# Kernel tuning notes

Hardware: AMD Instinct MI355X
Metric: run time of the kernel (lower is better)

## Reference

```python
import jax, jax.numpy as jnp
import numpy as np

N_NODES = 50000
N_EDGES = 800000
MUL = 32      # node feature multiplicity (32x0e)
A = 8         # node attr multiplicity (8x0e)
VE = 4        # edge attr multiplicity (4x0e)
FC_IN = 16    # edge_scalars dim (fc_neurons[0])
FC_H = 64     # fc hidden (fc_neurons[1])
W_NUMEL = MUL * VE  # tp.weight_numel for 'uvu' instruction = 128
NUM_NEIGHBORS = 16
N_LAYERS = 2


def fctp(x, y, w):
    # FullyConnectedTensorProduct on pure scalars: x[n,U], y[n,V], w[U,V,K]
    U, V = w.shape[0], w.shape[1]
    return jnp.einsum('nu,nv,uvk->nk', x, y, w) / np.float32(np.sqrt(U * V))


def tp_uvu(x, y, w):
    # 'uvu' TensorProduct with per-edge weights: x[e,U], y[e,V], w[e,U,V]
    V = y.shape[1]
    return jnp.einsum('eu,ev,euv->eu', x, y, w) / np.float32(np.sqrt(V))


def conv_layer(node_in, node_attr, edge_src, edge_dst, edge_attr, edge_scalars,
               sc_w, lin1_w, lin2_w, alpha_w, sce_w, fc_w0, fc_w1):
    n_nodes = node_in.shape[0]
    # per-edge weight generation (FullyConnectedNet with sin activation)
    h = jnp.sin(edge_scalars @ fc_w0 / np.float32(np.sqrt(FC_IN)))          # [E, FC_H]
    w = (h @ fc_w1 / np.float32(np.sqrt(FC_H))).reshape(-1, MUL, VE)        # [E, MUL, VE]
    # self connection + lin1
    node_sc = fctp(node_in, node_attr, sc_w)                                # [N, K]
    x = fctp(node_in, node_attr, lin1_w)                                    # [N, MUL]
    # gather -> tensor product -> scatter-add
    edge_features = tp_uvu(x[edge_src], edge_attr, w)                       # [E, MUL]
    node_features = jax.ops.segment_sum(edge_features, edge_dst,
                                        num_segments=n_nodes)
    node_features = node_features / np.float32(np.sqrt(NUM_NEIGHBORS))      # [N, MUL]
    node_conv = fctp(node_features, node_attr, lin2_w)                      # [N, K]
    alpha = fctp(node_features, node_attr, alpha_w)                         # [N, 1]
    # output_mask is all ones for scalar outputs -> alpha = 1 - 1 + alpha*1
    node_out = node_sc + alpha * node_conv
    edge_out = edge_attr + fctp(edge_features, edge_attr, sce_w) / np.float32(np.sqrt(NUM_NEIGHBORS))
    return node_out, edge_out


def setup_inputs() -> dict:
    key = jax.random.key(0)
    ks = jax.random.split(key, 13)
    L = N_LAYERS
    return {
        'node_features': jax.random.normal(ks[0], (N_NODES, MUL), jnp.float32),
        'node_attr':     jax.random.normal(ks[1], (N_NODES, A), jnp.float32),
        'edge_src':      jax.random.randint(ks[2], (N_EDGES,), 0, N_NODES),
        'edge_dst':      jax.random.randint(ks[3], (N_EDGES,), 0, N_NODES),
        'edge_attr':     jax.random.normal(ks[4], (N_EDGES, VE), jnp.float32),
        'edge_scalars':  jax.random.normal(ks[5], (N_EDGES, FC_IN), jnp.float32),
        # stacked per-layer parameters
        'sc_w':    jax.random.normal(ks[6],  (L, MUL, A, MUL), jnp.float32),
        'lin1_w':  jax.random.normal(ks[7],  (L, MUL, A, MUL), jnp.float32),
        'lin2_w':  jax.random.normal(ks[8],  (L, MUL, A, MUL), jnp.float32),
        'alpha_w': 0.1 * jax.random.normal(ks[9], (L, MUL, A, 1), jnp.float32),
        'sce_w':   jax.random.normal(ks[10], (L, MUL, VE, VE), jnp.float32),
        'fc_w0':   jax.random.normal(ks[11], (L, FC_IN, FC_H), jnp.float32),
        'fc_w1':   jax.random.normal(ks[12], (L, FC_H, W_NUMEL), jnp.float32),
    }


def reference(node_features, node_attr, edge_src, edge_dst, edge_attr, edge_scalars,
              sc_w, lin1_w, lin2_w, alpha_w, sce_w, fc_w0, fc_w1):
    nf, ea = node_features, edge_attr
    for l in range(N_LAYERS):
        nf, ea = conv_layer(nf, node_attr, edge_src, edge_dst, ea, edge_scalars,
                            sc_w[l], lin1_w[l], lin2_w[l], alpha_w[l],
                            sce_w[l], fc_w0[l], fc_w1[l])
        if l < N_LAYERS - 1:
            nf = jnp.sin(nf)  # Gate over even scalars == elementwise sin
    return nf, ea
```

## Files before the change

### kernel.cpp

```cpp
#include <hip/hip_runtime.h>
#include <hip/hip_bf16.h>


namespace {
constexpr int NN = 50000;
constexpr int NE = 800000;
constexpr int SCAN_BLOCKS = 196;

constexpr long OFF_NF   = 0;
constexpr long OFF_W0P  = 1600000;
constexpr long OFF_W2P  = 1602048;
constexpr long OFF_WNP  = 1610240;
constexpr long OFF_OFF  = 1638912;
constexpr long OFF_CUR  = 1688913;
constexpr long OFF_PERM = 1738913;
constexpr long OFF_BSUM = 2538913;
constexpr long OFF_EF   = 2539172;
}

typedef __attribute__((ext_vector_type(8))) short short8;
typedef __attribute__((ext_vector_type(4))) float f32x4;
typedef __attribute__((ext_vector_type(2))) float f32x2;
typedef f32x2 __attribute__((may_alias)) f32x2a;
typedef unsigned int   __attribute__((may_alias)) u32a;
typedef unsigned short __attribute__((may_alias)) u16a;
typedef float          __attribute__((may_alias)) f32a;

__device__ __forceinline__ float us2f(unsigned int u) {
    unsigned int x = u << 16; float f;
    __builtin_memcpy(&f, &x, sizeof(f));
    return f;
}
__device__ __forceinline__ unsigned short f2us(float f) {
    __hip_bfloat16 h = __float2bfloat16(f);
    unsigned short s;
    __builtin_memcpy(&s, &h, sizeof(s));
    return s;
}
__device__ __forceinline__ f32x2 mk2(float a, float b) {
    f32x2 r; r[0] = a; r[1] = b; return r;
}
__device__ __forceinline__ f32x2 pkfma(f32x2 a, f32x2 b, f32x2 c) {
#if __has_builtin(__builtin_elementwise_fma)
    return __builtin_elementwise_fma(a, b, c);
#else
    f32x2 r; r[0] = fmaf(a[0], b[0], c[0]); r[1] = fmaf(a[1], b[1], c[1]);
    return r;
#endif
}

__global__ __launch_bounds__(256) void k_hist(
        const int* __restrict__ dst, int* __restrict__ cnt,
        const float* __restrict__ f0, const float* __restrict__ f1,
        const float* __restrict__ l1w, const float* __restrict__ scw,
        const float* __restrict__ l2w, const float* __restrict__ aw,
        unsigned short* __restrict__ w0p, unsigned short* __restrict__ w2p,
        unsigned short* __restrict__ wnp) {
    int i = blockIdx.x * 256 + threadIdx.x;
    if (i < NE) atomicAdd(&cnt[dst[i]], 1);
    if (i < 4096) {
        int l = i >> 11, r = i & 2047;
        int nt = r >> 9, lane = (r >> 3) & 63, ii = r & 7;
        int k = (lane >> 4) * 8 + ii;
        int j = nt * 16 + (lane & 15);
        float v = (k < 16) ? 0.25f * f0[l * 1024 + k * 64 + j] : 0.f;
        w0p[i] = f2us(v);
    }
    if (i < 16384) {
        int l = i >> 13, r = i & 8191;
        int g = r >> 9;
        int kt = g >> 1, nt = g & 1;
        int lane = (r >> 3) & 63, ii = r & 7;
        int K = kt * 32 + (lane >> 4) * 8 + ii;
        int j = K >> 2, v = K & 3;
        int u = nt * 16 + (lane & 15);
        w2p[i] = f2us(f1[l * 8192 + j * 128 + u * 4 + v]);
    }
    if (i < 57344) {
        int l = i / 28672, r = i % 28672;
        int tile = r >> 12;
        int r2 = r & 4095;
        int kt = r2 >> 9, lane = (r2 >> 3) & 63, ii = r2 & 7;
        int k = kt * 32 + (lane >> 4) * 8 + ii;
        int u = k >> 3, v = k & 7;
        int col = lane & 15;
        int uvb = l * 8192 + (u * 8 + v) * 32;
        float val;
        if (tile < 2)      val = l1w[uvb + tile * 16 + col];
        else if (tile < 4) val = scw[uvb + (tile - 2) * 16 + col];
        else if (tile < 6) val = l2w[uvb + (tile - 4) * 16 + col];
        else               val = (col == 0) ? aw[l * 256 + u * 8 + v] : 0.f;
        wnp[i] = f2us(val);
    }
}

__global__ __launch_bounds__(256) void k_scan1(const int* __restrict__ cnt,
                                               int* __restrict__ bsum) {
    __shared__ int s[256];
    int t = threadIdx.x;
    int i = blockIdx.x * 256 + t;
    s[t] = (i < NN) ? cnt[i] : 0;
    __syncthreads();
    for (int d = 128; d > 0; d >>= 1) {
        if (t < d) s[t] += s[t + d];
        __syncthreads();
    }
    if (t == 0) bsum[blockIdx.x] = s[0];
}

__global__ __launch_bounds__(256) void k_scan2(int* __restrict__ bsum) {
    __shared__ int s[256];
    int t = threadIdx.x;
    int v = (t < SCAN_BLOCKS) ? bsum[t] : 0;
    s[t] = v; __syncthreads();
    for (int d = 1; d < 256; d <<= 1) {
        int x = (t >= d) ? s[t - d] : 0;
        __syncthreads();
        s[t] += x;
        __syncthreads();
    }
    if (t < SCAN_BLOCKS) bsum[t] = s[t] - v;
}

__global__ __launch_bounds__(256) void k_scan3(
        const int* __restrict__ cnt, const int* __restrict__ bsum,
        int* __restrict__ off, int* __restrict__ cur) {
    __shared__ int s[256];
    int t = threadIdx.x;
    int i = blockIdx.x * 256 + t;
    int v = (i < NN) ? cnt[i] : 0;
    s[t] = v; __syncthreads();
    for (int d = 1; d < 256; d <<= 1) {
        int x = (t >= d) ? s[t - d] : 0;
        __syncthreads();
        s[t] += x;
        __syncthreads();
    }
    int excl = s[t] - v + bsum[blockIdx.x];
    if (i < NN) { off[i] = excl; cur[i] = excl; }
    if (i == NN - 1) off[NN] = excl + v;
}

__global__ void k_perm(const int* __restrict__ dst, int* __restrict__ cur,
                       int* __restrict__ perm) {
    int e = blockIdx.x * 256 + threadIdx.x;
    if (e >= NE) return;
    perm[e] = atomicAdd(&cur[dst[e]], 1);
}

__device__ __forceinline__ void stage_xy_wl(const float* __restrict__ nf,
                                            const float* __restrict__ nattr,
                                            long n0, int w, int lane,
                                            f32a* Xs, f32a* Ys) {
    {
        int row = w * 16 + (lane >> 2), u = (lane & 3) * 8;
        long e = (n0 + row) * 32 + u;
        f32a* d = &Xs[row * 33 + u];
        if (e + 8 <= (long)NN * 32) {
            const float4* p = (const float4*)(nf + e);
            float4 q0 = p[0], q1 = p[1];
            d[0]=q0.x; d[1]=q0.y; d[2]=q0.z; d[3]=q0.w;
            d[4]=q1.x; d[5]=q1.y; d[6]=q1.z; d[7]=q1.w;
        } else {
#pragma unroll
            for (int i = 0; i < 8; i++)
                d[i] = (e + i < (long)NN * 32) ? nf[e + i] : 0.f;
        }
    }
    if (lane < 32) {
        int row = w * 16 + (lane >> 1), v = (lane & 1) * 4;
        long e = (n0 + row) * 8 + v;
        f32a* d = &Ys[row * 9 + v];
        if (e + 4 <= (long)NN * 8) {
            float4 q = *(const float4*)(nattr + e);
            d[0]=q.x; d[1]=q.y; d[2]=q.z; d[3]=q.w;
        } else {
#pragma unroll
            for (int i = 0; i < 4; i++)
                d[i] = (e + i < (long)NN * 8) ? nattr[e + i] : 0.f;
        }
    }
}

__global__ __launch_bounds__(256) void k_npre_m(
        const float* __restrict__ nf, const float* __restrict__ nattr,
        const unsigned short* __restrict__ wnp_l, float* __restrict__ xl) {
    __shared__ f32a Xs[64 * 33];
    __shared__ f32a Ys[64 * 9];
    const int t = threadIdx.x;
    const int lane = t & 63, w = t >> 6;
    const long n0 = (long)blockIdx.x * 64;
    stage_xy_wl(nf, nattr, n0, w, lane, Xs, Ys);
    __builtin_amdgcn_wave_barrier();

    const int l15 = lane & 15, quad = lane >> 4;
    const int nb = w * 16;
    float y[8], xk[8];
#pragma unroll
    for (int v = 0; v < 8; v++) y[v] = Ys[(nb + l15) * 9 + v];
#pragma unroll
    for (int kt = 0; kt < 8; kt++) xk[kt] = Xs[(nb + l15) * 33 + kt * 4 + quad];

    f32x4 a0, a1;
    a0[0]=0.f;a0[1]=0.f;a0[2]=0.f;a0[3]=0.f;
    a1[0]=0.f;a1[1]=0.f;a1[2]=0.f;a1[3]=0.f;
#pragma unroll
    for (int kt = 0; kt < 8; kt++) {
        float xv = xk[kt];
        short8 a;
#pragma unroll
        for (int i = 0; i < 8; i++) a[i] = (short)f2us(xv * y[i]);
        const short8 b0 = *(const short8*)(wnp_l + ((0 * 8 + kt) * 512) + lane * 8);
        const short8 b1 = *(const short8*)(wnp_l + ((1 * 8 + kt) * 512) + lane * 8);
        a0 = __builtin_amdgcn_mfma_f32_16x16x32_bf16(a, b0, a0, 0, 0, 0);
        a1 = __builtin_amdgcn_mfma_f32_16x16x32_bf16(a, b1, a1, 0, 0, 0);
    }
#pragma unroll
    for (int r = 0; r < 4; r++) {
        long n = n0 + nb + quad * 4 + r;
        if (n < NN) {
            xl[n * 32 + l15]      = a0[r] * 0.0625f;
            xl[n * 32 + 16 + l15] = a1[r] * 0.0625f;
        }
    }
}

__global__ __launch_bounds__(256) void k_edge_w(
        const float* __restrict__ esc, const int* __restrict__ srcp,
        const int* __restrict__ perm, const float* __restrict__ ea_in,
        float* __restrict__ ea_out, const float* __restrict__ xl,
        const unsigned short* __restrict__ w0p,
        const unsigned short* __restrict__ w2p,
        const float* __restrict__ sew, unsigned short* __restrict__ ef_bf) {
    __shared__ __align__(16) unsigned char SCR[4][8704];

    const int t = threadIdx.x;
    const int w = t >> 6, lane = t & 63;
    const int l15 = lane & 15, quad = lane >> 4;
    const long e0 = ((long)blockIdx.x * 4 + w) * 64;
    u16a* Hs = (u16a*)SCR[w];
    f32a* Ts = (f32a*)SCR[w];

    const long ge = e0 + lane;
    const int src = srcp[ge];
    const int pm  = perm[ge];
    const float4 ea3 = ((const float4*)ea_in)[ge];
    float4 eaq[4];
#pragma unroll
    for (int mt = 0; mt < 4; mt++)
        eaq[mt] = ((const float4*)ea_in)[e0 + mt * 16 + l15];

    short8 bw0[4];
#pragma unroll
    for (int nt = 0; nt < 4; nt++)
        bw0[nt] = *(const short8*)(w0p + (nt * 64 + lane) * 8);
#pragma unroll
    for (int mt = 0; mt < 4; mt++) {
        int row = mt * 16 + l15;
        short8 a;
#pragma unroll
        for (int i = 0; i < 8; i++) a[i] = 0;
        if (quad < 2) {
            const float4* ep = (const float4*)(esc + (e0 + row) * 16 + quad * 8);
            float4 p0 = ep[0], p1 = ep[1];
            a[0]=(short)f2us(p0.x); a[1]=(short)f2us(p0.y);
            a[2]=(short)f2us(p0.z); a[3]=(short)f2us(p0.w);
            a[4]=(short)f2us(p1.x); a[5]=(short)f2us(p1.y);
            a[6]=(short)f2us(p1.z); a[7]=(short)f2us(p1.w);
        }
#pragma unroll
        for (int nt = 0; nt < 4; nt++) {
            f32x4 c; c[0]=0.f; c[1]=0.f; c[2]=0.f; c[3]=0.f;
            c = __builtin_amdgcn_mfma_f32_16x16x32_bf16(a, bw0[nt], c, 0, 0, 0);
#pragma unroll
            for (int r = 0; r < 4; r++) {
                int edge = mt * 16 + quad * 4 + r;
                int j = nt * 16 + l15;
                Hs[edge * 68 + j] = f2us(__sinf(c[r]));
            }
        }
    }
    __builtin_amdgcn_wave_barrier();

    const float4* xp = (const float4*)(xl + (long)src * 32);
    float4 xq[8];
#pragma unroll
    for (int g = 0; g < 8; g++) xq[g] = xp[g];

    f32x4 acc[4][2];
#pragma unroll
    for (int mt = 0; mt < 4; mt++)
#pragma unroll
        for (int nt = 0; nt < 2; nt++) {
            acc[mt][nt][0]=0.f; acc[mt][nt][1]=0.f;
            acc[mt][nt][2]=0.f; acc[mt][nt][3]=0.f;
        }
#pragma unroll
    for (int kt = 0; kt < 8; kt++) {
        const short8 b0 = *(const short8*)(w2p + ((kt*2+0)*64 + lane) * 8);
        const short8 b1 = *(const short8*)(w2p + ((kt*2+1)*64 + lane) * 8);
#pragma unroll
        for (int mt = 0; mt < 4; mt++) {
            int row = mt * 16 + l15;
            unsigned int hp = *(const u32a*)(Hs + row * 68 + kt * 8 + quad * 2);
            float H0 = us2f(hp & 0xFFFFu), H1 = us2f(hp >> 16);
            float4 eav = eaq[mt];
            short8 a;
            a[0]=(short)f2us(H0*eav.x); a[1]=(short)f2us(H0*eav.y);
            a[2]=(short)f2us(H0*eav.z); a[3]=(short)f2us(H0*eav.w);
            a[4]=(short)f2us(H1*eav.x); a[5]=(short)f2us(H1*eav.y);
            a[6]=(short)f2us(H1*eav.z); a[7]=(short)f2us(H1*eav.w);
            acc[mt][0] = __builtin_amdgcn_mfma_f32_16x16x32_bf16(a, b0, acc[mt][0], 0, 0, 0);
            acc[mt][1] = __builtin_amdgcn_mfma_f32_16x16x32_bf16(a, b1, acc[mt][1], 0, 0, 0);
        }
    }
    __builtin_amdgcn_wave_barrier();

#pragma unroll
    for (int mt = 0; mt < 4; mt++)
#pragma unroll
        for (int nt = 0; nt < 2; nt++)
#pragma unroll
            for (int r = 0; r < 4; r++)
                Ts[(mt*16 + quad*4 + r) * 34 + nt*16 + l15] = acc[mt][nt][r] * 0.0625f;
    __builtin_amdgcn_wave_barrier();

    {
        f32x2 tvp[16];
#pragma unroll
        for (int i = 0; i < 16; i++)
            tvp[i] = *(const f32x2a*)(Ts + lane * 34 + i * 2);
        f32x2 efp[16];
#pragma unroll
        for (int g = 0; g < 8; g++) {
            float4 xv = xq[g];
            efp[2*g]   = mk2(xv.x, xv.y) * tvp[2*g];
            efp[2*g+1] = mk2(xv.z, xv.w) * tvp[2*g+1];
        }
        uint4* efo = (uint4*)(ef_bf + (long)pm * 32);
#pragma unroll
        for (int g = 0; g < 4; g++) {
            uint4 wv;
            wv.x = (unsigned)f2us(efp[4*g+0][0]) | ((unsigned)f2us(efp[4*g+0][1]) << 16);
            wv.y = (unsigned)f2us(efp[4*g+1][0]) | ((unsigned)f2us(efp[4*g+1][1]) << 16);
            wv.z = (unsigned)f2us(efp[4*g+2][0]) | ((unsigned)f2us(efp[4*g+2][1]) << 16);
            wv.w = (unsigned)f2us(efp[4*g+3][0]) | ((unsigned)f2us(efp[4*g+3][1]) << 16);
            efo[g] = wv;
        }
        float ea[4] = {ea3.x, ea3.y, ea3.z, ea3.w};
        f32x2 eo01 = {0.f, 0.f}, eo23 = {0.f, 0.f};
#pragma unroll
        for (int u = 0; u < 32; u++) {
            float efu = efp[u >> 1][u & 1];
#pragma unroll
            for (int v = 0; v < 4; v++) {
                float p = efu * ea[v];
                f32x2 pp = mk2(p, p);
                const f32x2 s01 = *(const f32x2a*)(sew + (u * 4 + v) * 4);
                const f32x2 s23 = *(const f32x2a*)(sew + (u * 4 + v) * 4 + 2);
                eo01 = pkfma(pp, s01, eo01);
                eo23 = pkfma(pp, s23, eo23);
            }
        }
        constexpr float SCE_SCALE = 0.02209708691f;
        float4 o;
        o.x = ea3.x + eo01[0] * SCE_SCALE;
        o.y = ea3.y + eo01[1] * SCE_SCALE;
        o.z = ea3.z + eo23[0] * SCE_SCALE;
        o.w = ea3.w + eo23[1] * SCE_SCALE;
        ((float4*)ea_out)[ge] = o;
    }
}

__global__ __launch_bounds__(256) void k_gpost_m(
        const int* __restrict__ off, const unsigned short* __restrict__ ef,
        const float* __restrict__ nf_cur, const float* __restrict__ nattr,
        const unsigned short* __restrict__ wnp_l,
        float* __restrict__ nf_next, float* __restrict__ out_nf, int last) {
    __shared__ f32a Xs[64 * 33];
    __shared__ f32a As[64 * 33];
    __shared__ f32a Ys[64 * 9];
    const int t = threadIdx.x;
    const int lane = t & 63, w = t >> 6;
    const long n0 = (long)blockIdx.x * 64;
    stage_xy_wl(nf_cur, nattr, n0, w, lane, Xs, Ys);

    {
        int g = (lane >> 2) & 1, l4 = lane & 3;
#pragma unroll
        for (int batch = 0; batch < 2; batch++) {
            int nl = w * 16 + batch * 8 + (lane >> 3);
            long n = n0 + nl;
            float v[8] = {0.f,0.f,0.f,0.f,0.f,0.f,0.f,0.f};
            if (n < NN) {
                int b = off[n] + g, en = off[n + 1];
                for (int r = b; r < en; r += 2) {
                    uint4 q = *(const uint4*)(ef + (long)r * 32 + l4 * 8);
                    v[0] += us2f(q.x & 0xFFFFu); v[1] += us2f(q.x >> 16);
                    v[2] += us2f(q.y & 0xFFFFu); v[3] += us2f(q.y >> 16);
                    v[4] += us2f(q.z & 0xFFFFu); v[5] += us2f(q.z >> 16);
                    v[6] += us2f(q.w & 0xFFFFu); v[7] += us2f(q.w >> 16);
                }
            }
#pragma unroll
            for (int i = 0; i < 8; i++) v[i] += __shfl_xor(v[i], 4);
            if (g == 0) {
#pragma unroll
                for (int i = 0; i < 8; i++)
                    As[nl * 33 + l4 * 8 + i] = v[i] * 0.25f;
            }
        }
    }
    __builtin_amdgcn_wave_barrier();

    const int l15 = lane & 15, quad = lane >> 4;
    const int nb = w * 16;
    float y[8], xk[8], ak[8];
#pragma unroll
    for (int v = 0; v < 8; v++) y[v] = Ys[(nb + l15) * 9 + v];
#pragma unroll
    for (int kt = 0; kt < 8; kt++) {
        xk[kt] = Xs[(nb + l15) * 33 + kt * 4 + quad];
        ak[kt] = As[(nb + l15) * 33 + kt * 4 + quad];
    }
    f32x4 sc0, sc1, l20, l21, al;
    sc0[0]=0.f;sc0[1]=0.f;sc0[2]=0.f;sc0[3]=0.f;
    sc1 = sc0; l20 = sc0; l21 = sc0; al = sc0;
#pragma unroll
    for (int kt = 0; kt < 8; kt++) {
        float xv = xk[kt], av = ak[kt];
        short8 ax, ag;
#pragma unroll
        for (int i = 0; i < 8; i++) {
            ax[i] = (short)f2us(xv * y[i]);
            ag[i] = (short)f2us(av * y[i]);
        }
        const short8 b2 = *(const short8*)(wnp_l + ((2 * 8 + kt) * 512) + lane * 8);
        const short8 b3 = *(const short8*)(wnp_l + ((3 * 8 + kt) * 512) + lane * 8);
        const short8 b4 = *(const short8*)(wnp_l + ((4 * 8 + kt) * 512) + lane * 8);
        const short8 b5 = *(const short8*)(wnp_l + ((5 * 8 + kt) * 512) + lane * 8);
        const short8 b6 = *(const short8*)(wnp_l + ((6 * 8 + kt) * 512) + lane * 8);
        sc0 = __builtin_amdgcn_mfma_f32_16x16x32_bf16(ax, b2, sc0, 0, 0, 0);
        sc1 = __builtin_amdgcn_mfma_f32_16x16x32_bf16(ax, b3, sc1, 0, 0, 0);
        l20 = __builtin_amdgcn_mfma_f32_16x16x32_bf16(ag, b4, l20, 0, 0, 0);
        l21 = __builtin_amdgcn_mfma_f32_16x16x32_bf16(ag, b5, l21, 0, 0, 0);
        al  = __builtin_amdgcn_mfma_f32_16x16x32_bf16(ag, b6, al,  0, 0, 0);
    }
#pragma unroll
    for (int r = 0; r < 4; r++) {
        float alpha = __shfl(al[r], quad * 16) * 0.0625f;
        long n = n0 + nb + quad * 4 + r;
        if (n < NN) {
            float o0 = sc0[r] * 0.0625f + alpha * (l20[r] * 0.0625f);
            float o1 = sc1[r] * 0.0625f + alpha * (l21[r] * 0.0625f);
            if (last) {
                out_nf[n * 32 + l15]      = o0;
                out_nf[n * 32 + 16 + l15] = o1;
            } else {
                nf_next[n * 32 + l15]      = __sinf(o0);
                nf_next[n * 32 + 16 + l15] = __sinf(o1);
            }
        }
    }
}

extern "C" void kernel_launch(void* const* d_in, const int* in_sizes, int n_in,
                              void* d_out, int out_size, void* d_ws, size_t ws_size,
                              hipStream_t stream) {
    int I_nf, I_na, I_esrc, I_edst, I_ea, I_esc, I_sc, I_l1, I_l2, I_al, I_se, I_f0, I_f1;
    if (in_sizes[0] == 1600000) {
        I_nf=0; I_na=1; I_esrc=2; I_edst=3; I_ea=4; I_esc=5;
        I_sc=6; I_l1=7; I_l2=8; I_al=9; I_se=10; I_f0=11; I_f1=12;
    } else {
        I_al=0; I_ea=1; I_edst=2; I_esc=3; I_esrc=4; I_f0=5; I_f1=6;
        I_l1=7; I_l2=8; I_na=9; I_nf=10; I_sc=11; I_se=12;
    }
    const float* nf_in = (const float*)d_in[I_nf];
    const float* na    = (const float*)d_in[I_na];
    const int*   esrc  = (const int*)d_in[I_esrc];
    const int*   edst  = (const int*)d_in[I_edst];
    const float* ea_in = (const float*)d_in[I_ea];
    const float* escl  = (const float*)d_in[I_esc];
    const float* w_sc  = (const float*)d_in[I_sc];
    const float* w_l1  = (const float*)d_in[I_l1];
    const float* w_l2  = (const float*)d_in[I_l2];
    const float* w_al  = (const float*)d_in[I_al];
    const float* w_se  = (const float*)d_in[I_se];
    const float* w_f0  = (const float*)d_in[I_f0];
    const float* w_f1  = (const float*)d_in[I_f1];

    float* ws = (float*)d_ws;
    float* out_nf = (float*)d_out;
    float* out_ea = out_nf + (long)NN * 32;

    unsigned short* w0p     = (unsigned short*)(ws + OFF_W0P);
    unsigned short* w2p     = (unsigned short*)(ws + OFF_W2P);
    unsigned short* wnp     = (unsigned short*)(ws + OFF_WNP);
    int*            csr_off = (int*)(ws + OFF_OFF);
    int*            csr_cur = (int*)(ws + OFF_CUR);
    int*            perm    = (int*)(ws + OFF_PERM);
    int*            bsum    = (int*)(ws + OFF_BSUM);
    unsigned short* ef_bf   = (unsigned short*)(ws + OFF_EF);

    hipMemsetAsync(csr_cur, 0, NN * sizeof(int), stream);
    k_hist<<<3125, 256, 0, stream>>>(edst, csr_cur, w_f0, w_f1,
                                     w_l1, w_sc, w_l2, w_al, w0p, w2p, wnp);
    k_scan1<<<SCAN_BLOCKS, 256, 0, stream>>>(csr_cur, bsum);
    k_scan2<<<1, 256, 0, stream>>>(bsum);
    k_scan3<<<SCAN_BLOCKS, 256, 0, stream>>>(csr_cur, bsum, csr_off, csr_cur);
    k_perm<<<3125, 256, 0, stream>>>(edst, csr_cur, perm);

    for (int l = 0; l < 2; l++) {
        int last = (l == 1);
        const float* nf_cur = (l == 0) ? nf_in : (ws + OFF_NF);
        const float* ea_cur = (l == 0) ? ea_in : out_ea;

        k_npre_m<<<782, 256, 0, stream>>>(nf_cur, na, wnp + l * 28672,
                                          out_nf );
        k_edge_w<<<3125, 256, 0, stream>>>(escl, esrc, perm, ea_cur, out_ea,
                                           out_nf , w0p + l * 2048,
                                           w2p + l * 8192, w_se + l * 512,
                                           ef_bf);
        k_gpost_m<<<782, 256, 0, stream>>>(csr_off, ef_bf,
                                           nf_cur, na, wnp + l * 28672,
                                           ws + OFF_NF, out_nf, last);
    }
}
```

Before: 380.7 us.

## Fuse next layer's lin1 node projection into gather-post kernel; widen segment reduction

The layer-1 node pre-projection (lin1 via MFMA) is now computed at the end of the layer-0 gather/post kernel from the freshly computed sin outputs kept in shared memory, so the separate k_npre_m launch and its re-read of node features are dropped for layer 1. The CSR segment sum also splits each node's edges across 4 lane groups instead of 2, with an extra shuffle reduction, to raise parallelism in the gather. The cost is extra MFMA work and register pressure in the post kernel.

Result: no change. 379.1 us (-0.4%).

```diff
diff --git a/kernel.cpp b/kernel.cpp
--- a/kernel.cpp
+++ b/kernel.cpp
@@ -376,7 +376,9 @@
         const int* __restrict__ off, const unsigned short* __restrict__ ef,
         const float* __restrict__ nf_cur, const float* __restrict__ nattr,
         const unsigned short* __restrict__ wnp_l,
-        float* __restrict__ nf_next, float* __restrict__ out_nf, int last) {
+        float* __restrict__ nf_next, float* __restrict__ out_nf, int last,
+        const unsigned short* __restrict__ wnp_next,
+        float* __restrict__ xl_out) {
     __shared__ f32a Xs[64 * 33];
     __shared__ f32a As[64 * 33];
     __shared__ f32a Ys[64 * 9];
@@ -386,15 +388,15 @@
     stage_xy_wl(nf_cur, nattr, n0, w, lane, Xs, Ys);
 
     {
-        int g = (lane >> 2) & 1, l4 = lane & 3;
-#pragma unroll
-        for (int batch = 0; batch < 2; batch++) {
-            int nl = w * 16 + batch * 8 + (lane >> 3);
+        int g = (lane >> 2) & 3, l4 = lane & 3;
+#pragma unroll
+        for (int batch = 0; batch < 4; batch++) {
+            int nl = w * 16 + batch * 4 + (lane >> 4);
             long n = n0 + nl;
             float v[8] = {0.f,0.f,0.f,0.f,0.f,0.f,0.f,0.f};
             if (n < NN) {
                 int b = off[n] + g, en = off[n + 1];
-                for (int r = b; r < en; r += 2) {
+                for (int r = b; r < en; r += 4) {
                     uint4 q = *(const uint4*)(ef + (long)r * 32 + l4 * 8);
                     v[0] += us2f(q.x & 0xFFFFu); v[1] += us2f(q.x >> 16);
                     v[2] += us2f(q.y & 0xFFFFu); v[3] += us2f(q.y >> 16);
@@ -403,7 +405,10 @@
                 }
             }
 #pragma unroll
-            for (int i = 0; i < 8; i++) v[i] += __shfl_xor(v[i], 4);
+            for (int i = 0; i < 8; i++) {
+                v[i] += __shfl_xor(v[i], 4);
+                v[i] += __shfl_xor(v[i], 8);
+            }
             if (g == 0) {
 #pragma unroll
                 for (int i = 0; i < 8; i++)
@@ -450,15 +455,49 @@
     for (int r = 0; r < 4; r++) {
         float alpha = __shfl(al[r], quad * 16) * 0.0625f;
         long n = n0 + nb + quad * 4 + r;
-        if (n < NN) {
-            float o0 = sc0[r] * 0.0625f + alpha * (l20[r] * 0.0625f);
-            float o1 = sc1[r] * 0.0625f + alpha * (l21[r] * 0.0625f);
-            if (last) {
+        float o0 = sc0[r] * 0.0625f + alpha * (l20[r] * 0.0625f);
+        float o1 = sc1[r] * 0.0625f + alpha * (l21[r] * 0.0625f);
+        if (last) {
+            if (n < NN) {
                 out_nf[n * 32 + l15]      = o0;
                 out_nf[n * 32 + 16 + l15] = o1;
-            } else {
-                nf_next[n * 32 + l15]      = __sinf(o0);
-                nf_next[n * 32 + 16 + l15] = __sinf(o1);
+            }
+        } else {
+            float t0 = __sinf(o0), t1 = __sinf(o1);
+            if (n < NN) {
+                nf_next[n * 32 + l15]      = t0;
+                nf_next[n * 32 + 16 + l15] = t1;
+            }
+            Xs[(nb + quad * 4 + r) * 33 + l15]      = t0;
+            Xs[(nb + quad * 4 + r) * 33 + 16 + l15] = t1;
+        }
+    }
+    if (!last) {
+        __builtin_amdgcn_wave_barrier();
+        float xk2[8];
+#pragma unroll
+        for (int kt = 0; kt < 8; kt++)
+            xk2[kt] = Xs[(nb + l15) * 33 + kt * 4 + quad];
+        f32x4 a0, a1;
+        a0[0]=0.f;a0[1]=0.f;a0[2]=0.f;a0[3]=0.f;
+        a1 = a0;
+#pragma unroll
+        for (int kt = 0; kt < 8; kt++) {
+            float xv = xk2[kt];
+            short8 a;
+#pragma unroll
+            for (int i = 0; i < 8; i++) a[i] = (short)f2us(xv * y[i]);
+            const short8 b0 = *(const short8*)(wnp_next + ((0 * 8 + kt) * 512) + lane * 8);
+            const short8 b1 = *(const short8*)(wnp_next + ((1 * 8 + kt) * 512) + lane * 8);
+            a0 = __builtin_amdgcn_mfma_f32_16x16x32_bf16(a, b0, a0, 0, 0, 0);
+            a1 = __builtin_amdgcn_mfma_f32_16x16x32_bf16(a, b1, a1, 0, 0, 0);
+        }
+#pragma unroll
+        for (int r = 0; r < 4; r++) {
+            long n = n0 + nb + quad * 4 + r;
+            if (n < NN) {
+                xl_out[n * 32 + l15]      = a0[r] * 0.0625f;
+                xl_out[n * 32 + 16 + l15] = a1[r] * 0.0625f;
             }
         }
     }
@@ -515,14 +554,17 @@
         const float* nf_cur = (l == 0) ? nf_in : (ws + OFF_NF);
         const float* ea_cur = (l == 0) ? ea_in : out_ea;
 
-        k_npre_m<<<782, 256, 0, stream>>>(nf_cur, na, wnp + l * 28672,
-                                          out_nf );
+        if (l == 0)
+            k_npre_m<<<782, 256, 0, stream>>>(nf_cur, na, wnp,
+                                              out_nf );
         k_edge_w<<<3125, 256, 0, stream>>>(escl, esrc, perm, ea_cur, out_ea,
                                            out_nf , w0p + l * 2048,
                                            w2p + l * 8192, w_se + l * 512,
                                            ef_bf);
         k_gpost_m<<<782, 256, 0, stream>>>(csr_off, ef_bf,
                                            nf_cur, na, wnp + l * 28672,
-                                           ws + OFF_NF, out_nf, last);
-    }
-}
+                                           ws + OFF_NF, out_nf, last,
+                                           wnp + 28672 ,
+                                           out_nf );
+    }
+}
```
